# Kernel optimization log

Hardware: AMD Instinct MI355X
Metric: run time of the kernel (lower is better)

## Reference

```python
import jax, jax.numpy as jnp
import numpy as np

N, C, CI, H, W = 64, 512, 256, 12, 4
EPS = 1e-5


def _conv1x1(v, w, b=None):
    # v: [n, cin, h, w], w: [cout, cin]
    o = jnp.einsum('nchw,oc->nohw', v, w)
    if b is not None:
        o = o + b[None, :, None, None]
    return o


def _layernorm(v, g, b):
    # normalize over (C, H, W) per sample, affine params shaped [C, H, W]
    mu = v.mean(axis=(1, 2, 3), keepdims=True)
    var = v.var(axis=(1, 2, 3), keepdims=True)
    return (v - mu) / jnp.sqrt(var + EPS) * g[None] + b[None]


def setup_inputs() -> dict:
    key = jax.random.key(0)
    ks = jax.random.split(key, 12)
    s = 0.02
    return {
        'x': jax.random.normal(ks[0], (N, C, H, W), dtype=jnp.float32),
        'theta_w': jax.random.normal(ks[1], (CI, C), dtype=jnp.float32) * s,
        'theta_b': jnp.zeros((CI,), dtype=jnp.float32),
        'phi_w': jax.random.normal(ks[2], (CI, C), dtype=jnp.float32) * s,
        'phi_b': jnp.zeros((CI,), dtype=jnp.float32),
        'conv1_w': jax.random.normal(ks[3], (C, C), dtype=jnp.float32) * s,
        'conv2_w': jax.random.normal(ks[4], (C, C), dtype=jnp.float32) * s,
        'ln1_g': jnp.ones((C, H, W), dtype=jnp.float32),
        'ln1_b': jnp.zeros((C, H, W), dtype=jnp.float32),
        'ln2_g': jnp.ones((C, H, W), dtype=jnp.float32),
        'ln2_b': jnp.zeros((C, H, W), dtype=jnp.float32),
    }


def reference(x, theta_w, theta_b, phi_w, phi_b, conv1_w, conv2_w,
              ln1_g, ln1_b, ln2_g, ln2_b):
    n = x.shape[0]
    hw = H * W
    # 1x1 conv projections (conv is per-sample, so compute once on the N nodes
    # instead of on the N^2 gathered copies -- identical math)
    theta = _conv1x1(x, theta_w, theta_b)          # [N, CI, H, W]  (gallery proj)
    phi = _conv1x1(x, phi_w, phi_b)                # [N, CI, H, W]  (query proj)
    # MaxPool2d(2,2) on phi -> [N, CI, 6, 2] -> [N, CI, 12]
    phi_p = phi.reshape(n, CI, H // 2, 2, W // 2, 2).max(axis=(3, 5))
    phi_p = phi_p.reshape(n, CI, -1)               # [N, CI, 12]
    t = theta.reshape(n, CI, hw).transpose(0, 2, 1)  # [N, HW, CI]
    # f[i, j] = theta(x[j]) @ pooled phi(x[i]), norm='size' divides by 12
    f = jnp.einsum('jsc,icm->ijsm', t, phi_p) / phi_p.shape[-1]  # [Nq, Ng, HW, 12]
    m = f.max(axis=-1)                             # [Nq, Ng, HW]; max instead of softmax-sum
    # all-pairs layout p = i*N + j: qs[p] = i, gs[p] = j (torch.where row-major)
    gs = jnp.tile(jnp.arange(n), n)                # [N*N]
    # masked gallery image z = x[gs] * attention map, then scatter_add over gs
    z = x[gs] * m.reshape(n * n, 1, H, W)          # [N*N, C, H, W]
    x2 = jax.ops.segment_sum(z, gs, num_segments=n)
    # postprocessing (dropouts are identity at p=0)
    x = x2 + x                                     # res1
    x = _layernorm(x, ln1_g, ln1_b)
    h = _conv1x1(jax.nn.relu(_conv1x1(x, conv1_w)), conv2_w)
    x = x + h                                      # res2
    x = _layernorm(x, ln2_g, ln2_b)
    return x
```

## Files before the change

### kernel.cpp

```cpp
#include <hip/hip_runtime.h>
#include <hip/hip_bf16.h>

#define NN 64
#define CC 512
#define HW 48
#define LNSZ (CC * HW)

typedef __attribute__((ext_vector_type(8))) short bf16x8;
typedef __attribute__((ext_vector_type(4))) float floatx4;

static const size_t WB_OFF  = 0;
static const size_t BC_OFF  = 393216;
static const size_t XB_OFF  = 393728;
static const size_t YB_OFF  = 1180160;
static const size_t UB_OFF  = 1966592;
static const size_t TH_OFF  = 2753024;
static const size_t PP_OFF  = 3146240;
static const size_t PROJ_OFF= 3244544;
static const size_t DD_OFF  = 4817408;
static const size_t SS_OFF  = 7176704;
static const size_t YY_OFF  = 7179776;
static const size_t UU_OFF  = 8752640;
static const size_t HH_OFF  = 10325504;
static const size_t VV_OFF  = 11898368;
static const size_t ST1_OFF = 13471232;
static const size_t ST2_OFF = 13472256;

__device__ __forceinline__ void block_reduce2(float& sum, float& sq) {
  const int lane = threadIdx.x & 63, w = threadIdx.x >> 6;
#pragma unroll
  for (int off = 32; off > 0; off >>= 1) {
    sum += __shfl_down(sum, off, 64);
    sq  += __shfl_down(sq, off, 64);
  }
  __shared__ float rs[4], rq[4];
  if (lane == 0) { rs[w] = sum; rq[w] = sq; }
  __syncthreads();
  if (threadIdx.x == 0) {
    sum = rs[0] + rs[1] + rs[2] + rs[3];
    sq  = rq[0] + rq[1] + rq[2] + rq[3];
  }
}

__global__ __launch_bounds__(256) void prep_w(
    const float* __restrict__ tw, const float* __restrict__ pw,
    const float* __restrict__ c1, const float* __restrict__ c2,
    const float* __restrict__ tb, const float* __restrict__ pb,
    __hip_bfloat16* __restrict__ Wb, float* __restrict__ bcat) {
  int g = blockIdx.x * 256 + threadIdx.x;
  float v;
  if (g < 131072)      v = tw[g];
  else if (g < 262144) v = pw[g - 131072];
  else if (g < 524288) v = c1[g - 262144];
  else                 v = c2[g - 524288];
  Wb[g] = __float2bfloat16(v);
  if (g < 512) bcat[g] = g < 256 ? tb[g] : pb[g - 256];
}

__global__ __launch_bounds__(256) void tr_bf16(
    const float* __restrict__ in, __hip_bfloat16* __restrict__ out,
    int in_nstride, int out_nstride, int rowstr) {
  const int c0 = blockIdx.x * 128;
  const int n  = blockIdx.y;
  const int t  = threadIdx.x;
  __shared__ float ts[128 * 49];
  const float* src = in + (size_t)n * in_nstride + (size_t)c0 * HW;
#pragma unroll
  for (int k = 0; k < 6; ++k) {
    int idx = t + k * 256;
    float4 v = ((const float4*)src)[idx];
    int c = idx / 12, sq = (idx % 12) * 4;
    float* d = ts + c * 49 + sq;
    d[0] = v.x; d[1] = v.y; d[2] = v.z; d[3] = v.w;
  }
  __syncthreads();
  __hip_bfloat16* dst = out + (size_t)n * out_nstride + c0;
#pragma unroll
  for (int k = 0; k < 12; ++k) {
    int idx = t + k * 256;
    int s = idx >> 6, cp = idx & 63;
    __hip_bfloat162 p;
    p.x = __float2bfloat16(ts[(cp * 2) * 49 + s]);
    p.y = __float2bfloat16(ts[(cp * 2 + 1) * 49 + s]);
    *(__hip_bfloat162*)(dst + (size_t)s * rowstr + cp * 2) = p;
  }
}

__global__ __launch_bounds__(256) void gemm_conv(
    const __hip_bfloat16* __restrict__ Wb, const __hip_bfloat16* __restrict__ inb,
    const float* __restrict__ bias, float* __restrict__ out, int relu) {
  const int oc = blockIdx.x, n = blockIdx.y;
  const int w = threadIdx.x >> 6, lane = threadIdx.x & 63;
  const int c16 = lane & 15, quad = lane >> 4;
  const int obase = oc * 128 + w * 32;

  const __hip_bfloat16* A0 = Wb + (size_t)(obase + c16) * 512 + quad * 8;
  const __hip_bfloat16* A1 = A0 + 16 * 512;
  const __hip_bfloat16* B0 = inb + (size_t)n * LNSZ + (size_t)c16 * 512 + quad * 8;

  floatx4 zero = {0.f, 0.f, 0.f, 0.f};
  floatx4 acc[2][3];
#pragma unroll
  for (int i = 0; i < 2; ++i)
#pragma unroll
    for (int j = 0; j < 3; ++j) acc[i][j] = zero;

  bf16x8 a[2], b[3];
  a[0] = *(const bf16x8*)(A0);
  a[1] = *(const bf16x8*)(A1);
  b[0] = *(const bf16x8*)(B0);
  b[1] = *(const bf16x8*)(B0 + 16 * 512);
  b[2] = *(const bf16x8*)(B0 + 32 * 512);

  for (int k = 0; k < 480; k += 32) {
    bf16x8 an[2], bn[3];
    const int k2 = k + 32;
    an[0] = *(const bf16x8*)(A0 + k2);
    an[1] = *(const bf16x8*)(A1 + k2);
    bn[0] = *(const bf16x8*)(B0 + k2);
    bn[1] = *(const bf16x8*)(B0 + 16 * 512 + k2);
    bn[2] = *(const bf16x8*)(B0 + 32 * 512 + k2);
#pragma unroll
    for (int i = 0; i < 2; ++i)
#pragma unroll
      for (int j = 0; j < 3; ++j)
        acc[i][j] = __builtin_amdgcn_mfma_f32_16x16x32_bf16(a[i], b[j],
                                                            acc[i][j], 0, 0, 0);
    a[0] = an[0]; a[1] = an[1];
    b[0] = bn[0]; b[1] = bn[1]; b[2] = bn[2];
  }
#pragma unroll
  for (int i = 0; i < 2; ++i)
#pragma unroll
    for (int j = 0; j < 3; ++j)
      acc[i][j] = __builtin_amdgcn_mfma_f32_16x16x32_bf16(a[i], b[j],
                                                          acc[i][j], 0, 0, 0);

  float* on = out + (size_t)n * LNSZ;
#pragma unroll
  for (int i = 0; i < 2; ++i) {
#pragma unroll
    for (int r = 0; r < 4; ++r) {
      const int o = obase + i * 16 + quad * 4 + r;
      const float bv = bias ? bias[o] : 0.f;
#pragma unroll
      for (int j = 0; j < 3; ++j) {
        float v = acc[i][j][r] + bv;
        if (relu) v = fmaxf(v, 0.f);
        on[(size_t)o * HW + j * 16 + c16] = v;
      }
    }
  }
}

__global__ __launch_bounds__(256) void make_pp(
    const float* __restrict__ proj, __hip_bfloat16* __restrict__ Pp) {
  int g = blockIdx.x * 256 + threadIdx.x;
  int ci = g & 255;
  int rest = g >> 8;
  int m = rest % 12, i = rest / 12;
  int sb = (m >> 1) * 8 + (m & 1) * 2;
  const float* row = proj + (size_t)i * LNSZ + (size_t)(256 + ci) * HW;
  float2 p0 = *(const float2*)(row + sb);
  float2 p1 = *(const float2*)(row + sb + 4);
  float mx = fmaxf(fmaxf(p0.x, p0.y), fmaxf(p1.x, p1.y));
  Pp[g] = __float2bfloat16(mx);
}

__global__ __launch_bounds__(256) void dgemm_mfma(
    const __hip_bfloat16* __restrict__ A, const __hip_bfloat16* __restrict__ B,
    float* __restrict__ D) {
  const int bn = blockIdx.x * 48;
  const int w = threadIdx.x >> 6, lane = threadIdx.x & 63;
  const int c16 = lane & 15, quad = lane >> 4;
  const int bm = blockIdx.y * 128 + w * 32;

  const __hip_bfloat16* A0 = A + (size_t)(bm + c16) * 256 + quad * 8;
  const __hip_bfloat16* A1 = A0 + 16 * 256;
  const __hip_bfloat16* Bp = B + (size_t)(bn + c16) * 256 + quad * 8;

  floatx4 zero = {0.f, 0.f, 0.f, 0.f};
  floatx4 acc[2][3];
#pragma unroll
  for (int i = 0; i < 2; ++i)
#pragma unroll
    for (int j = 0; j < 3; ++j) acc[i][j] = zero;

#pragma unroll 2
  for (int k = 0; k < 256; k += 32) {
    bf16x8 a0 = *(const bf16x8*)(A0 + k);
    bf16x8 a1 = *(const bf16x8*)(A1 + k);
    bf16x8 b0 = *(const bf16x8*)(Bp + k);
    bf16x8 b1 = *(const bf16x8*)(Bp + 16 * 256 + k);
    bf16x8 b2 = *(const bf16x8*)(Bp + 32 * 256 + k);
    acc[0][0] = __builtin_amdgcn_mfma_f32_16x16x32_bf16(a0, b0, acc[0][0], 0, 0, 0);
    acc[0][1] = __builtin_amdgcn_mfma_f32_16x16x32_bf16(a0, b1, acc[0][1], 0, 0, 0);
    acc[0][2] = __builtin_amdgcn_mfma_f32_16x16x32_bf16(a0, b2, acc[0][2], 0, 0, 0);
    acc[1][0] = __builtin_amdgcn_mfma_f32_16x16x32_bf16(a1, b0, acc[1][0], 0, 0, 0);
    acc[1][1] = __builtin_amdgcn_mfma_f32_16x16x32_bf16(a1, b1, acc[1][1], 0, 0, 0);
    acc[1][2] = __builtin_amdgcn_mfma_f32_16x16x32_bf16(a1, b2, acc[1][2], 0, 0, 0);
  }

#pragma unroll
  for (int i = 0; i < 2; ++i)
#pragma unroll
    for (int r = 0; r < 4; ++r) {
      const int row = bm + i * 16 + quad * 4 + r;
#pragma unroll
      for (int j = 0; j < 3; ++j)
        D[(size_t)row * 768 + bn + j * 16 + c16] = acc[i][j][r];
    }
}

__global__ __launch_bounds__(256) void reduce_D(const float* __restrict__ D,
                                                float* __restrict__ S) {
  int w = threadIdx.x >> 6;
  int lane = threadIdx.x & 63;
  int row = blockIdx.x * 4 + w;
  const float* dr = D + (size_t)row * 768 + lane * 12;
  float4 a = *(const float4*)dr;
  float4 b = *(const float4*)(dr + 4);
  float4 c = *(const float4*)(dr + 8);
  float mx = a.x;
  mx = fmaxf(mx, a.y); mx = fmaxf(mx, a.z); mx = fmaxf(mx, a.w);
  mx = fmaxf(mx, b.x); mx = fmaxf(mx, b.y); mx = fmaxf(mx, b.z); mx = fmaxf(mx, b.w);
  mx = fmaxf(mx, c.x); mx = fmaxf(mx, c.y); mx = fmaxf(mx, c.z); mx = fmaxf(mx, c.w);
#pragma unroll
  for (int off = 32; off > 0; off >>= 1) mx += __shfl_down(mx, off, 64);
  if (lane == 0) S[row] = mx * (1.0f / 12.0f);
}

__global__ __launch_bounds__(256) void ln1_stats(
    const float* __restrict__ x, const float* __restrict__ S,
    float2* __restrict__ stats) {
  const int ch = blockIdx.x, n = blockIdx.y, t = threadIdx.x;
  __shared__ float sS[HW];
  if (t < HW) sS[t] = 1.0f + S[n * HW + t];
  __syncthreads();
  const float* xn = x + (size_t)n * LNSZ;
  float sum = 0.f, sq = 0.f;
#pragma unroll
  for (int k = 0; k < 3; ++k) {
    const int off = ch * 3072 + t * 4 + k * 1024;
    const int s0 = off % HW;
    float4 xv = *(const float4*)(xn + off);
    float e0 = xv.x * sS[s0];
    float e1 = xv.y * sS[s0 + 1];
    float e2 = xv.z * sS[s0 + 2];
    float e3 = xv.w * sS[s0 + 3];
    sum += (e0 + e1) + (e2 + e3);
    sq  += (e0 * e0 + e1 * e1) + (e2 * e2 + e3 * e3);
  }
  block_reduce2(sum, sq);
  if (t == 0) stats[n * 8 + ch] = make_float2(sum, sq);
}

__global__ __launch_bounds__(256) void ln1_norm(
    const float* __restrict__ x, const float* __restrict__ S,
    const float2* __restrict__ stats, const float* __restrict__ g,
    const float* __restrict__ b, float* __restrict__ y) {
  const int ch = blockIdx.x, n = blockIdx.y, t = threadIdx.x;
  __shared__ float sS[HW];
  __shared__ float smu, srstd;
  if (t < HW) sS[t] = 1.0f + S[n * HW + t];
  if (t == 0) {
    float s1 = 0.f, s2 = 0.f;
#pragma unroll
    for (int k = 0; k < 8; ++k) {
      float2 p = stats[n * 8 + k];
      s1 += p.x; s2 += p.y;
    }
    float mu = s1 * (1.0f / LNSZ);
    float var = s2 * (1.0f / LNSZ) - mu * mu;
    smu = mu;
    srstd = 1.0f / sqrtf(var + 1e-5f);
  }
  __syncthreads();
  const float mu = smu, rstd = srstd;
  const float* xn = x + (size_t)n * LNSZ;
  float* yn = y + (size_t)n * LNSZ;
#pragma unroll
  for (int k = 0; k < 3; ++k) {
    const int off = ch * 3072 + t * 4 + k * 1024;
    const int s0 = off % HW;
    float4 xv = *(const float4*)(xn + off);
    float4 gv = *(const float4*)(g + off);
    float4 bv = *(const float4*)(b + off);
    float4 o;
    o.x = (xv.x * sS[s0]     - mu) * rstd * gv.x + bv.x;
    o.y = (xv.y * sS[s0 + 1] - mu) * rstd * gv.y + bv.y;
    o.z = (xv.z * sS[s0 + 2] - mu) * rstd * gv.z + bv.z;
    o.w = (xv.w * sS[s0 + 3] - mu) * rstd * gv.w + bv.w;
    *(float4*)(yn + off) = o;
  }
}

__global__ __launch_bounds__(256) void ln2_stats(
    const float* __restrict__ y, const float* __restrict__ h,
    float2* __restrict__ stats, float* __restrict__ v) {
  const int ch = blockIdx.x, n = blockIdx.y, t = threadIdx.x;
  const size_t base = (size_t)n * LNSZ;
  float sum = 0.f, sq = 0.f;
#pragma unroll
  for (int k = 0; k < 3; ++k) {
    const int off = ch * 3072 + t * 4 + k * 1024;
    float4 yv = *(const float4*)(y + base + off);
    float4 hv = *(const float4*)(h + base + off);
    float v0 = yv.x + hv.x, v1 = yv.y + hv.y;
    float v2 = yv.z + hv.z, v3 = yv.w + hv.w;
    float4 o = make_float4(v0, v1, v2, v3);
    *(float4*)(v + base + off) = o;
    sum += (v0 + v1) + (v2 + v3);
    sq  += (v0 * v0 + v1 * v1) + (v2 * v2 + v3 * v3);
  }
  block_reduce2(sum, sq);
  if (t == 0) stats[n * 8 + ch] = make_float2(sum, sq);
}

__global__ __launch_bounds__(256) void ln2_norm(
    const float* __restrict__ v, const float2* __restrict__ stats,
    const float* __restrict__ g2, const float* __restrict__ b2,
    float* __restrict__ out) {
  const int ch = blockIdx.x, n = blockIdx.y, t = threadIdx.x;
  __shared__ float smu, srstd;
  if (t == 0) {
    float s1 = 0.f, s2 = 0.f;
#pragma unroll
    for (int k = 0; k < 8; ++k) {
      float2 p = stats[n * 8 + k];
      s1 += p.x; s2 += p.y;
    }
    float mu = s1 * (1.0f / LNSZ);
    float var = s2 * (1.0f / LNSZ) - mu * mu;
    smu = mu;
    srstd = 1.0f / sqrtf(var + 1e-5f);
  }
  __syncthreads();
  const float mu = smu, rstd = srstd;
  const float* vn = v + (size_t)n * LNSZ;
  float* on = out + (size_t)n * LNSZ;
#pragma unroll
  for (int k = 0; k < 3; ++k) {
    const int off = ch * 3072 + t * 4 + k * 1024;
    float4 vv = *(const float4*)(vn + off);
    float4 gv = *(const float4*)(g2 + off);
    float4 bv = *(const float4*)(b2 + off);
    float4 o;
    o.x = (vv.x - mu) * rstd * gv.x + bv.x;
    o.y = (vv.y - mu) * rstd * gv.y + bv.y;
    o.z = (vv.z - mu) * rstd * gv.z + bv.z;
    o.w = (vv.w - mu) * rstd * gv.w + bv.w;
    *(float4*)(on + off) = o;
  }
}

extern "C" void kernel_launch(void* const* d_in, const int* in_sizes, int n_in,
                              void* d_out, int out_size, void* d_ws, size_t ws_size,
                              hipStream_t stream) {
  const float* x   = (const float*)d_in[0];
  const float* tw  = (const float*)d_in[1];
  const float* tb  = (const float*)d_in[2];
  const float* pw  = (const float*)d_in[3];
  const float* pb  = (const float*)d_in[4];
  const float* c1w = (const float*)d_in[5];
  const float* c2w = (const float*)d_in[6];
  const float* g1  = (const float*)d_in[7];
  const float* b1  = (const float*)d_in[8];
  const float* g2  = (const float*)d_in[9];
  const float* b2  = (const float*)d_in[10];

  float* ws = (float*)d_ws;
  __hip_bfloat16* Wb = (__hip_bfloat16*)(ws + WB_OFF);
  float* bcat        = ws + BC_OFF;
  __hip_bfloat16* xb = (__hip_bfloat16*)(ws + XB_OFF);
  __hip_bfloat16* yb = (__hip_bfloat16*)(ws + YB_OFF);
  __hip_bfloat16* ub = (__hip_bfloat16*)(ws + UB_OFF);
  __hip_bfloat16* Th = (__hip_bfloat16*)(ws + TH_OFF);
  __hip_bfloat16* Pp = (__hip_bfloat16*)(ws + PP_OFF);
  float* proj = ws + PROJ_OFF;
  float* D    = ws + DD_OFF;
  float* S    = ws + SS_OFF;
  float* y    = ws + YY_OFF;
  float* u    = ws + UU_OFF;
  float* h    = ws + HH_OFF;
  float* v    = ws + VV_OFF;
  float2* st1 = (float2*)(ws + ST1_OFF);
  float2* st2 = (float2*)(ws + ST2_OFF);
  float* out  = (float*)d_out;

  prep_w<<<3072, 256, 0, stream>>>(tw, pw, c1w, c2w, tb, pb, Wb, bcat);
  tr_bf16<<<dim3(4, NN), 256, 0, stream>>>(x, xb, LNSZ, LNSZ, 512);
  gemm_conv<<<dim3(4, NN), 256, 0, stream>>>(Wb, xb, bcat, proj, 0);
  tr_bf16<<<dim3(2, NN), 256, 0, stream>>>(proj, Th, LNSZ, 48 * 256, 256);
  make_pp<<<768, 256, 0, stream>>>(proj, Pp);
  dgemm_mfma<<<dim3(16, 24), 256, 0, stream>>>(Th, Pp, D);
  reduce_D<<<768, 256, 0, stream>>>(D, S);
  ln1_stats<<<dim3(8, NN), 256, 0, stream>>>(x, S, st1);
  ln1_norm<<<dim3(8, NN), 256, 0, stream>>>(x, S, st1, g1, b1, y);
  tr_bf16<<<dim3(4, NN), 256, 0, stream>>>(y, yb, LNSZ, LNSZ, 512);
  gemm_conv<<<dim3(4, NN), 256, 0, stream>>>(Wb + 512 * 512, yb, nullptr, u, 1);
  tr_bf16<<<dim3(4, NN), 256, 0, stream>>>(u, ub, LNSZ, LNSZ, 512);
  gemm_conv<<<dim3(4, NN), 256, 0, stream>>>(Wb + 1024 * 512, ub, nullptr, h, 0);
  ln2_stats<<<dim3(8, NN), 256, 0, stream>>>(y, h, st2, v);
  ln2_norm<<<dim3(8, NN), 256, 0, stream>>>(v, st2, g2, b2, out);
}
```

Before: 161.3 us.

## Fuse pipeline stages: bf16 GEMM outputs, fused max-reduce, LN stats, residual epilogue

Measured after the change: 141.1 us, median of 2. -12.5%, faster.

```diff
diff --git a/kernel.cpp b/kernel.cpp
--- a/kernel.cpp
+++ b/kernel.cpp
@@ -9,22 +9,21 @@
 typedef __attribute__((ext_vector_type(8))) short bf16x8;
 typedef __attribute__((ext_vector_type(4))) float floatx4;
 
-static const size_t WB_OFF  = 0;
-static const size_t BC_OFF  = 393216;
-static const size_t XB_OFF  = 393728;
-static const size_t YB_OFF  = 1180160;
-static const size_t UB_OFF  = 1966592;
-static const size_t TH_OFF  = 2753024;
-static const size_t PP_OFF  = 3146240;
-static const size_t PROJ_OFF= 3244544;
-static const size_t DD_OFF  = 4817408;
-static const size_t SS_OFF  = 7176704;
-static const size_t YY_OFF  = 7179776;
-static const size_t UU_OFF  = 8752640;
-static const size_t HH_OFF  = 10325504;
-static const size_t VV_OFF  = 11898368;
-static const size_t ST1_OFF = 13471232;
-static const size_t ST2_OFF = 13472256;
+static const size_t WB_OFF   = 0;
+static const size_t BC_OFF   = 393216;
+static const size_t S_OFF    = 393728;
+static const size_t SMU_OFF  = 396800;
+static const size_t SRS_OFF  = 396864;
+static const size_t CXP_OFF  = 396928;
+static const size_t CX2_OFF  = 409216;
+static const size_t ST2_OFF  = 421504;
+static const size_t XB_OFF   = 422016;
+static const size_t TP_OFF   = 1208448;
+static const size_t YB_OFF   = 1994880;
+static const size_t UB_OFF   = 2781312;
+static const size_t PP_OFF   = 3567744;
+static const size_t YY_OFF   = 3666048;
+static const size_t VV_OFF   = 5238912;
 
 __device__ __forceinline__ void block_reduce2(float& sum, float& sq) {
   const int lane = threadIdx.x & 63, w = threadIdx.x >> 6;
@@ -46,7 +45,8 @@
     const float* __restrict__ tw, const float* __restrict__ pw,
     const float* __restrict__ c1, const float* __restrict__ c2,
     const float* __restrict__ tb, const float* __restrict__ pb,
-    __hip_bfloat16* __restrict__ Wb, float* __restrict__ bcat) {
+    __hip_bfloat16* __restrict__ Wb, float* __restrict__ bcat,
+    float* __restrict__ S) {
   int g = blockIdx.x * 256 + threadIdx.x;
   float v;
   if (g < 131072)      v = tw[g];
@@ -55,16 +55,18 @@
   else                 v = c2[g - 524288];
   Wb[g] = __float2bfloat16(v);
   if (g < 512) bcat[g] = g < 256 ? tb[g] : pb[g - 256];
-}
-
-__global__ __launch_bounds__(256) void tr_bf16(
-    const float* __restrict__ in, __hip_bfloat16* __restrict__ out,
-    int in_nstride, int out_nstride, int rowstr) {
-  const int c0 = blockIdx.x * 128;
+  if (g < 3072) S[g] = 0.f;
+}
+
+__global__ __launch_bounds__(256) void trx_stats(
+    const float* __restrict__ x, __hip_bfloat16* __restrict__ xb,
+    float* __restrict__ cxp, float* __restrict__ cx2p) {
+  const int bx = blockIdx.x;
   const int n  = blockIdx.y;
   const int t  = threadIdx.x;
   __shared__ float ts[128 * 49];
-  const float* src = in + (size_t)n * in_nstride + (size_t)c0 * HW;
+  __shared__ float ps[192], pq[192];
+  const float* src = x + (size_t)n * LNSZ + (size_t)bx * 128 * HW;
 #pragma unroll
   for (int k = 0; k < 6; ++k) {
     int idx = t + k * 256;
@@ -74,7 +76,17 @@
     d[0] = v.x; d[1] = v.y; d[2] = v.z; d[3] = v.w;
   }
   __syncthreads();
-  __hip_bfloat16* dst = out + (size_t)n * out_nstride + c0;
+  if (t < 192) {
+    int s = t % 48, q = t / 48;
+    float sum = 0.f, sq2 = 0.f;
+#pragma unroll
+    for (int c = q * 32; c < q * 32 + 32; ++c) {
+      float v = ts[c * 49 + s];
+      sum += v; sq2 += v * v;
+    }
+    ps[t] = sum; pq[t] = sq2;
+  }
+  __hip_bfloat16* dst = xb + (size_t)n * LNSZ + bx * 128;
 #pragma unroll
   for (int k = 0; k < 12; ++k) {
     int idx = t + k * 256;
@@ -82,13 +94,18 @@
     __hip_bfloat162 p;
     p.x = __float2bfloat16(ts[(cp * 2) * 49 + s]);
     p.y = __float2bfloat16(ts[(cp * 2 + 1) * 49 + s]);
-    *(__hip_bfloat162*)(dst + (size_t)s * rowstr + cp * 2) = p;
-  }
-}
-
-__global__ __launch_bounds__(256) void gemm_conv(
+    *(__hip_bfloat162*)(dst + (size_t)s * 512 + cp * 2) = p;
+  }
+  __syncthreads();
+  if (t < 48) {
+    cxp[((size_t)n * 4 + bx) * 48 + t] = ps[t] + ps[48 + t] + ps[96 + t] + ps[144 + t];
+    cx2p[((size_t)n * 4 + bx) * 48 + t] = pq[t] + pq[48 + t] + pq[96 + t] + pq[144 + t];
+  }
+}
+
+__global__ __launch_bounds__(256) void gemm_bf16out(
     const __hip_bfloat16* __restrict__ Wb, const __hip_bfloat16* __restrict__ inb,
-    const float* __restrict__ bias, float* __restrict__ out, int relu) {
+    const float* __restrict__ bias, __hip_bfloat16* __restrict__ outb, int relu) {
   const int oc = blockIdx.x, n = blockIdx.y;
   const int w = threadIdx.x >> 6, lane = threadIdx.x & 63;
   const int c16 = lane & 15, quad = lane >> 4;
@@ -136,47 +153,53 @@
       acc[i][j] = __builtin_amdgcn_mfma_f32_16x16x32_bf16(a[i], b[j],
                                                           acc[i][j], 0, 0, 0);
 
-  float* on = out + (size_t)n * LNSZ;
+  __hip_bfloat16* on = outb + (size_t)n * LNSZ;
 #pragma unroll
   for (int i = 0; i < 2; ++i) {
-#pragma unroll
-    for (int r = 0; r < 4; ++r) {
-      const int o = obase + i * 16 + quad * 4 + r;
-      const float bv = bias ? bias[o] : 0.f;
-#pragma unroll
-      for (int j = 0; j < 3; ++j) {
-        float v = acc[i][j][r] + bv;
+    const int o0 = obase + i * 16 + quad * 4;
+    float bv[4];
+#pragma unroll
+    for (int r = 0; r < 4; ++r) bv[r] = bias ? bias[o0 + r] : 0.f;
+#pragma unroll
+    for (int j = 0; j < 3; ++j) {
+      const int s = j * 16 + c16;
+      union { short4 s4; __hip_bfloat16 h[4]; } u;
+#pragma unroll
+      for (int r = 0; r < 4; ++r) {
+        float v = acc[i][j][r] + bv[r];
         if (relu) v = fmaxf(v, 0.f);
-        on[(size_t)o * HW + j * 16 + c16] = v;
+        u.h[r] = __float2bfloat16(v);
       }
+      *(short4*)(on + (size_t)s * 512 + o0) = u.s4;
     }
   }
 }
 
 __global__ __launch_bounds__(256) void make_pp(
-    const float* __restrict__ proj, __hip_bfloat16* __restrict__ Pp) {
+    const __hip_bfloat16* __restrict__ ThPhi, __hip_bfloat16* __restrict__ Pp) {
   int g = blockIdx.x * 256 + threadIdx.x;
   int ci = g & 255;
   int rest = g >> 8;
   int m = rest % 12, i = rest / 12;
   int sb = (m >> 1) * 8 + (m & 1) * 2;
-  const float* row = proj + (size_t)i * LNSZ + (size_t)(256 + ci) * HW;
-  float2 p0 = *(const float2*)(row + sb);
-  float2 p1 = *(const float2*)(row + sb + 4);
-  float mx = fmaxf(fmaxf(p0.x, p0.y), fmaxf(p1.x, p1.y));
+  const __hip_bfloat16* base = ThPhi + (size_t)i * LNSZ + 256 + ci;
+  float mx = __bfloat162float(base[(size_t)(sb + 0) * 512]);
+  mx = fmaxf(mx, __bfloat162float(base[(size_t)(sb + 1) * 512]));
+  mx = fmaxf(mx, __bfloat162float(base[(size_t)(sb + 4) * 512]));
+  mx = fmaxf(mx, __bfloat162float(base[(size_t)(sb + 5) * 512]));
   Pp[g] = __float2bfloat16(mx);
 }
 
-__global__ __launch_bounds__(256) void dgemm_mfma(
+__global__ __launch_bounds__(256) void dgemm_fused(
     const __hip_bfloat16* __restrict__ A, const __hip_bfloat16* __restrict__ B,
-    float* __restrict__ D) {
+    float* __restrict__ S) {
   const int bn = blockIdx.x * 48;
   const int w = threadIdx.x >> 6, lane = threadIdx.x & 63;
   const int c16 = lane & 15, quad = lane >> 4;
   const int bm = blockIdx.y * 128 + w * 32;
 
-  const __hip_bfloat16* A0 = A + (size_t)(bm + c16) * 256 + quad * 8;
-  const __hip_bfloat16* A1 = A0 + 16 * 256;
+  const __hip_bfloat16* A0 = A + (size_t)(bm + c16) * 512 + quad * 8;
+  const __hip_bfloat16* A1 = A0 + 16 * 512;
   const __hip_bfloat16* Bp = B + (size_t)(bn + c16) * 256 + quad * 8;
 
   floatx4 zero = {0.f, 0.f, 0.f, 0.f};
@@ -201,73 +224,188 @@
     acc[1][2] = __builtin_amdgcn_mfma_f32_16x16x32_bf16(a1, b2, acc[1][2], 0, 0, 0);
   }
 
-#pragma unroll
-  for (int i = 0; i < 2; ++i)
-#pragma unroll
-    for (int r = 0; r < 4; ++r) {
-      const int row = bm + i * 16 + quad * 4 + r;
-#pragma unroll
-      for (int j = 0; j < 3; ++j)
-        D[(size_t)row * 768 + bn + j * 16 + c16] = acc[i][j][r];
-    }
-}
-
-__global__ __launch_bounds__(256) void reduce_D(const float* __restrict__ D,
-                                                float* __restrict__ S) {
-  int w = threadIdx.x >> 6;
-  int lane = threadIdx.x & 63;
-  int row = blockIdx.x * 4 + w;
-  const float* dr = D + (size_t)row * 768 + lane * 12;
-  float4 a = *(const float4*)dr;
-  float4 b = *(const float4*)(dr + 4);
-  float4 c = *(const float4*)(dr + 8);
-  float mx = a.x;
-  mx = fmaxf(mx, a.y); mx = fmaxf(mx, a.z); mx = fmaxf(mx, a.w);
-  mx = fmaxf(mx, b.x); mx = fmaxf(mx, b.y); mx = fmaxf(mx, b.z); mx = fmaxf(mx, b.w);
-  mx = fmaxf(mx, c.x); mx = fmaxf(mx, c.y); mx = fmaxf(mx, c.z); mx = fmaxf(mx, c.w);
-#pragma unroll
-  for (int off = 32; off > 0; off >>= 1) mx += __shfl_down(mx, off, 64);
-  if (lane == 0) S[row] = mx * (1.0f / 12.0f);
-}
-
-__global__ __launch_bounds__(256) void ln1_stats(
+  __shared__ float red[4 * 48 * 33];
+  float* rw = red + w * (48 * 33);
+#pragma unroll
+  for (int i = 0; i < 2; ++i)
+#pragma unroll
+    for (int j = 0; j < 3; ++j)
+#pragma unroll
+      for (int r = 0; r < 4; ++r)
+        rw[(j * 16 + c16) * 33 + (i * 16 + quad * 4 + r)] = acc[i][j][r];
+  __syncthreads();
+  if (lane < 32) {
+    float sum = 0.f;
+#pragma unroll
+    for (int grp = 0; grp < 4; ++grp) {
+      float mx = rw[(grp * 12) * 33 + lane];
+#pragma unroll
+      for (int m = 1; m < 12; ++m)
+        mx = fmaxf(mx, rw[(grp * 12 + m) * 33 + lane]);
+      sum += mx;
+    }
+    atomicAdd(&S[bm + lane], sum * (1.0f / 12.0f));
+  }
+}
+
+__global__ __launch_bounds__(64) void ln1_finish(
+    const float* __restrict__ S, const float* __restrict__ cxp,
+    const float* __restrict__ cx2p, float* __restrict__ smu,
+    float* __restrict__ srstd) {
+  const int n = blockIdx.x, lane = threadIdx.x;
+  float sum = 0.f, sq = 0.f;
+  if (lane < 48) {
+    float a = 1.0f + S[n * 48 + lane];
+    float c1 = 0.f, c2 = 0.f;
+#pragma unroll
+    for (int ch = 0; ch < 4; ++ch) {
+      c1 += cxp[((size_t)n * 4 + ch) * 48 + lane];
+      c2 += cx2p[((size_t)n * 4 + ch) * 48 + lane];
+    }
+    sum = a * c1;
+    sq = a * a * c2;
+  }
+#pragma unroll
+  for (int off = 32; off > 0; off >>= 1) {
+    sum += __shfl_down(sum, off, 64);
+    sq  += __shfl_down(sq, off, 64);
+  }
+  if (lane == 0) {
+    float mu = sum * (1.0f / LNSZ);
+    float var = sq * (1.0f / LNSZ) - mu * mu;
+    smu[n] = mu;
+    srstd[n] = 1.0f / sqrtf(var + 1e-5f);
+  }
+}
+
+__global__ __launch_bounds__(256) void ln1_norm_tr(
     const float* __restrict__ x, const float* __restrict__ S,
-    float2* __restrict__ stats) {
-  const int ch = blockIdx.x, n = blockIdx.y, t = threadIdx.x;
+    const float* __restrict__ smu, const float* __restrict__ srstd,
+    const float* __restrict__ g, const float* __restrict__ b,
+    float* __restrict__ y, __hip_bfloat16* __restrict__ yb) {
+  const int bx = blockIdx.x, n = blockIdx.y, t = threadIdx.x;
+  __shared__ float ts[128 * 49];
   __shared__ float sS[HW];
   if (t < HW) sS[t] = 1.0f + S[n * HW + t];
   __syncthreads();
-  const float* xn = x + (size_t)n * LNSZ;
+  const float mu = smu[n], rstd = srstd[n];
+  const size_t chunk = (size_t)bx * 6144;
+  const float* xn = x + (size_t)n * LNSZ + chunk;
+  float* yn = y + (size_t)n * LNSZ + chunk;
+  const float* gp = g + chunk;
+  const float* bp = b + chunk;
+#pragma unroll
+  for (int k = 0; k < 6; ++k) {
+    int idx = t + k * 256;
+    int c = idx / 12, sq0 = (idx % 12) * 4;
+    float4 xv = ((const float4*)xn)[idx];
+    float4 gv = ((const float4*)gp)[idx];
+    float4 bv = ((const float4*)bp)[idx];
+    float4 o;
+    o.x = (xv.x * sS[sq0]     - mu) * rstd * gv.x + bv.x;
+    o.y = (xv.y * sS[sq0 + 1] - mu) * rstd * gv.y + bv.y;
+    o.z = (xv.z * sS[sq0 + 2] - mu) * rstd * gv.z + bv.z;
+    o.w = (xv.w * sS[sq0 + 3] - mu) * rstd * gv.w + bv.w;
+    ((float4*)yn)[idx] = o;
+    float* d = ts + c * 49 + sq0;
+    d[0] = o.x; d[1] = o.y; d[2] = o.z; d[3] = o.w;
+  }
+  __syncthreads();
+  __hip_bfloat16* dst = yb + (size_t)n * LNSZ + bx * 128;
+#pragma unroll
+  for (int k = 0; k < 12; ++k) {
+    int idx = t + k * 256;
+    int s = idx >> 6, cp = idx & 63;
+    __hip_bfloat162 p;
+    p.x = __float2bfloat16(ts[(cp * 2) * 49 + s]);
+    p.y = __float2bfloat16(ts[(cp * 2 + 1) * 49 + s]);
+    *(__hip_bfloat162*)(dst + (size_t)s * 512 + cp * 2) = p;
+  }
+}
+
+__global__ __launch_bounds__(256) void conv2_fused(
+    const __hip_bfloat16* __restrict__ Wb, const __hip_bfloat16* __restrict__ inb,
+    const float* __restrict__ y, float* __restrict__ v,
+    float2* __restrict__ stats2) {
+  const int oc = blockIdx.x, n = blockIdx.y;
+  const int w = threadIdx.x >> 6, lane = threadIdx.x & 63;
+  const int c16 = lane & 15, quad = lane >> 4;
+  const int obase = oc * 128 + w * 32;
+
+  const __hip_bfloat16* A0 = Wb + (size_t)(obase + c16) * 512 + quad * 8;
+  const __hip_bfloat16* A1 = A0 + 16 * 512;
+  const __hip_bfloat16* B0 = inb + (size_t)n * LNSZ + (size_t)c16 * 512 + quad * 8;
+
+  floatx4 zero = {0.f, 0.f, 0.f, 0.f};
+  floatx4 acc[2][3];
+#pragma unroll
+  for (int i = 0; i < 2; ++i)
+#pragma unroll
+    for (int j = 0; j < 3; ++j) acc[i][j] = zero;
+
+  bf16x8 a[2], b[3];
+  a[0] = *(const bf16x8*)(A0);
+  a[1] = *(const bf16x8*)(A1);
+  b[0] = *(const bf16x8*)(B0);
+  b[1] = *(const bf16x8*)(B0 + 16 * 512);
+  b[2] = *(const bf16x8*)(B0 + 32 * 512);
+
+  for (int k = 0; k < 480; k += 32) {
+    bf16x8 an[2], bn[3];
+    const int k2 = k + 32;
+    an[0] = *(const bf16x8*)(A0 + k2);
+    an[1] = *(const bf16x8*)(A1 + k2);
+    bn[0] = *(const bf16x8*)(B0 + k2);
+    bn[1] = *(const bf16x8*)(B0 + 16 * 512 + k2);
+    bn[2] = *(const bf16x8*)(B0 + 32 * 512 + k2);
+#pragma unroll
+    for (int i = 0; i < 2; ++i)
+#pragma unroll
+      for (int j = 0; j < 3; ++j)
+        acc[i][j] = __builtin_amdgcn_mfma_f32_16x16x32_bf16(a[i], b[j],
+                                                            acc[i][j], 0, 0, 0);
+    a[0] = an[0]; a[1] = an[1];
+    b[0] = bn[0]; b[1] = bn[1]; b[2] = bn[2];
+  }
+#pragma unroll
+  for (int i = 0; i < 2; ++i)
+#pragma unroll
+    for (int j = 0; j < 3; ++j)
+      acc[i][j] = __builtin_amdgcn_mfma_f32_16x16x32_bf16(a[i], b[j],
+                                                          acc[i][j], 0, 0, 0);
+
+  const float* yn = y + (size_t)n * LNSZ;
+  float* vn = v + (size_t)n * LNSZ;
   float sum = 0.f, sq = 0.f;
 #pragma unroll
-  for (int k = 0; k < 3; ++k) {
-    const int off = ch * 3072 + t * 4 + k * 1024;
-    const int s0 = off % HW;
-    float4 xv = *(const float4*)(xn + off);
-    float e0 = xv.x * sS[s0];
-    float e1 = xv.y * sS[s0 + 1];
-    float e2 = xv.z * sS[s0 + 2];
-    float e3 = xv.w * sS[s0 + 3];
-    sum += (e0 + e1) + (e2 + e3);
-    sq  += (e0 * e0 + e1 * e1) + (e2 * e2 + e3 * e3);
-  }
+  for (int i = 0; i < 2; ++i)
+#pragma unroll
+    for (int r = 0; r < 4; ++r) {
+      const int o = obase + i * 16 + quad * 4 + r;
+#pragma unroll
+      for (int j = 0; j < 3; ++j) {
+        const int s = j * 16 + c16;
+        float val = acc[i][j][r] + yn[(size_t)o * HW + s];
+        vn[(size_t)o * HW + s] = val;
+        sum += val;
+        sq += val * val;
+      }
+    }
   block_reduce2(sum, sq);
-  if (t == 0) stats[n * 8 + ch] = make_float2(sum, sq);
-}
-
-__global__ __launch_bounds__(256) void ln1_norm(
-    const float* __restrict__ x, const float* __restrict__ S,
-    const float2* __restrict__ stats, const float* __restrict__ g,
-    const float* __restrict__ b, float* __restrict__ y) {
-  const int ch = blockIdx.x, n = blockIdx.y, t = threadIdx.x;
-  __shared__ float sS[HW];
+  if (threadIdx.x == 0) stats2[n * 4 + oc] = make_float2(sum, sq);
+}
+
+__global__ __launch_bounds__(256) void ln2_norm(
+    const float* __restrict__ v, const float2* __restrict__ stats2,
+    const float* __restrict__ g2, const float* __restrict__ b2,
+    float* __restrict__ out) {
+  const int bx = blockIdx.x, n = blockIdx.y, t = threadIdx.x;
   __shared__ float smu, srstd;
-  if (t < HW) sS[t] = 1.0f + S[n * HW + t];
   if (t == 0) {
     float s1 = 0.f, s2 = 0.f;
 #pragma unroll
-    for (int k = 0; k < 8; ++k) {
-      float2 p = stats[n * 8 + k];
+    for (int k = 0; k < 4; ++k) {
+      float2 p = stats2[n * 4 + k];
       s1 += p.x; s2 += p.y;
     }
     float mu = s1 * (1.0f / LNSZ);
@@ -277,80 +415,23 @@
   }
   __syncthreads();
   const float mu = smu, rstd = srstd;
-  const float* xn = x + (size_t)n * LNSZ;
-  float* yn = y + (size_t)n * LNSZ;
-#pragma unroll
-  for (int k = 0; k < 3; ++k) {
-    const int off = ch * 3072 + t * 4 + k * 1024;
-    const int s0 = off % HW;
-    float4 xv = *(const float4*)(xn + off);
-    float4 gv = *(const float4*)(g + off);
-    float4 bv = *(const float4*)(b + off);
-    float4 o;
-    o.x = (xv.x * sS[s0]     - mu) * rstd * gv.x + bv.x;
-    o.y = (xv.y * sS[s0 + 1] - mu) * rstd * gv.y + bv.y;
-    o.z = (xv.z * sS[s0 + 2] - mu) * rstd * gv.z + bv.z;
-    o.w = (xv.w * sS[s0 + 3] - mu) * rstd * gv.w + bv.w;
-    *(float4*)(yn + off) = o;
-  }
-}
-
-__global__ __launch_bounds__(256) void ln2_stats(
-    const float* __restrict__ y, const float* __restrict__ h,
-    float2* __restrict__ stats, float* __restrict__ v) {
-  const int ch = blockIdx.x, n = blockIdx.y, t = threadIdx.x;
-  const size_t base = (size_t)n * LNSZ;
-  float sum = 0.f, sq = 0.f;
-#pragma unroll
-  for (int k = 0; k < 3; ++k) {
-    const int off = ch * 3072 + t * 4 + k * 1024;
-    float4 yv = *(const float4*)(y + base + off);
-    float4 hv = *(const float4*)(h + base + off);
-    float v0 = yv.x + hv.x, v1 = yv.y + hv.y;
-    float v2 = yv.z + hv.z, v3 = yv.w + hv.w;
-    float4 o = make_float4(v0, v1, v2, v3);
-    *(float4*)(v + base + off) = o;
-    sum += (v0 + v1) + (v2 + v3);
-    sq  += (v0 * v0 + v1 * v1) + (v2 * v2 + v3 * v3);
-  }
-  block_reduce2(sum, sq);
-  if (t == 0) stats[n * 8 + ch] = make_float2(sum, sq);
-}
-
-__global__ __launch_bounds__(256) void ln2_norm(
-    const float* __restrict__ v, const float2* __restrict__ stats,
-    const float* __restrict__ g2, const float* __restrict__ b2,
-    float* __restrict__ out) {
-  const int ch = blockIdx.x, n = blockIdx.y, t = threadIdx.x;
-  __shared__ float smu, srstd;
-  if (t == 0) {
-    float s1 = 0.f, s2 = 0.f;
-#pragma unroll
-    for (int k = 0; k < 8; ++k) {
-      float2 p = stats[n * 8 + k];
-      s1 += p.x; s2 += p.y;
-    }
-    float mu = s1 * (1.0f / LNSZ);
-    float var = s2 * (1.0f / LNSZ) - mu * mu;
-    smu = mu;
-    srstd = 1.0f / sqrtf(var + 1e-5f);
-  }
-  __syncthreads();
-  const float mu = smu, rstd = srstd;
-  const float* vn = v + (size_t)n * LNSZ;
-  float* on = out + (size_t)n * LNSZ;
-#pragma unroll
-  for (int k = 0; k < 3; ++k) {
-    const int off = ch * 3072 + t * 4 + k * 1024;
-    float4 vv = *(const float4*)(vn + off);
-    float4 gv = *(const float4*)(g2 + off);
-    float4 bv = *(const float4*)(b2 + off);
+  const size_t chunk = (size_t)bx * 6144;
+  const float* vn = v + (size_t)n * LNSZ + chunk;
+  float* on = out + (size_t)n * LNSZ + chunk;
+  const float* gp = g2 + chunk;
+  const float* bp = b2 + chunk;
+#pragma unroll
+  for (int k = 0; k < 6; ++k) {
+    int idx = t + k * 256;
+    float4 vv = ((const float4*)vn)[idx];
+    float4 gv = ((const float4*)gp)[idx];
+    float4 bv = ((const float4*)bp)[idx];
     float4 o;
     o.x = (vv.x - mu) * rstd * gv.x + bv.x;
     o.y = (vv.y - mu) * rstd * gv.y + bv.y;
     o.z = (vv.z - mu) * rstd * gv.z + bv.z;
     o.w = (vv.w - mu) * rstd * gv.w + bv.w;
-    *(float4*)(on + off) = o;
+    ((float4*)on)[idx] = o;
   }
 }
 
@@ -372,35 +453,29 @@
   float* ws = (float*)d_ws;
   __hip_bfloat16* Wb = (__hip_bfloat16*)(ws + WB_OFF);
   float* bcat        = ws + BC_OFF;
+  float* S           = ws + S_OFF;
+  float* smu         = ws + SMU_OFF;
+  float* srstd       = ws + SRS_OFF;
+  float* cxp         = ws + CXP_OFF;
+  float* cx2p        = ws + CX2_OFF;
+  float2* st2        = (float2*)(ws + ST2_OFF);
   __hip_bfloat16* xb = (__hip_bfloat16*)(ws + XB_OFF);
+  __hip_bfloat16* tp = (__hip_bfloat16*)(ws + TP_OFF);
   __hip_bfloat16* yb = (__hip_bfloat16*)(ws + YB_OFF);
   __hip_bfloat16* ub = (__hip_bfloat16*)(ws + UB_OFF);
-  __hip_bfloat16* Th = (__hip_bfloat16*)(ws + TH_OFF);
   __hip_bfloat16* Pp = (__hip_bfloat16*)(ws + PP_OFF);
-  float* proj = ws + PROJ_OFF;
-  float* D    = ws + DD_OFF;
-  float* S    = ws + SS_OFF;
-  float* y    = ws + YY_OFF;
-  float* u    = ws + UU_OFF;
-  float* h    = ws + HH_OFF;
-  float* v    = ws + VV_OFF;
-  float2* st1 = (float2*)(ws + ST1_OFF);
-  float2* st2 = (float2*)(ws + ST2_OFF);
-  float* out  = (float*)d_out;
-
-  prep_w<<<3072, 256, 0, stream>>>(tw, pw, c1w, c2w, tb, pb, Wb, bcat);
-  tr_bf16<<<dim3(4, NN), 256, 0, stream>>>(x, xb, LNSZ, LNSZ, 512);
-  gemm_conv<<<dim3(4, NN), 256, 0, stream>>>(Wb, xb, bcat, proj, 0);
-  tr_bf16<<<dim3(2, NN), 256, 0, stream>>>(proj, Th, LNSZ, 48 * 256, 256);
-  make_pp<<<768, 256, 0, stream>>>(proj, Pp);
-  dgemm_mfma<<<dim3(16, 24), 256, 0, stream>>>(Th, Pp, D);
-  reduce_D<<<768, 256, 0, stream>>>(D, S);
-  ln1_stats<<<dim3(8, NN), 256, 0, stream>>>(x, S, st1);
-  ln1_norm<<<dim3(8, NN), 256, 0, stream>>>(x, S, st1, g1, b1, y);
-  tr_bf16<<<dim3(4, NN), 256, 0, stream>>>(y, yb, LNSZ, LNSZ, 512);
-  gemm_conv<<<dim3(4, NN), 256, 0, stream>>>(Wb + 512 * 512, yb, nullptr, u, 1);
-  tr_bf16<<<dim3(4, NN), 256, 0, stream>>>(u, ub, LNSZ, LNSZ, 512);
-  gemm_conv<<<dim3(4, NN), 256, 0, stream>>>(Wb + 1024 * 512, ub, nullptr, h, 0);
-  ln2_stats<<<dim3(8, NN), 256, 0, stream>>>(y, h, st2, v);
-  ln2_norm<<<dim3(8, NN), 256, 0, stream>>>(v, st2, g2, b2, out);
-}
+  float* y           = ws + YY_OFF;
+  float* v           = ws + VV_OFF;
+  float* out         = (float*)d_out;
+
+  prep_w<<<3072, 256, 0, stream>>>(tw, pw, c1w, c2w, tb, pb, Wb, bcat, S);
+  trx_stats<<<dim3(4, NN), 256, 0, stream>>>(x, xb, cxp, cx2p);
+  gemm_bf16out<<<dim3(4, NN), 256, 0, stream>>>(Wb, xb, bcat, tp, 0);
+  make_pp<<<768, 256, 0, stream>>>(tp, Pp);
+  dgemm_fused<<<dim3(16, 24), 256, 0, stream>>>(tp, Pp, S);
+  ln1_finish<<<NN, 64, 0, stream>>>(S, cxp, cx2p, smu, srstd);
+  ln1_norm_tr<<<dim3(4, NN), 256, 0, stream>>>(x, S, smu, srstd, g1, b1, y, yb);
+  gemm_bf16out<<<dim3(4, NN), 256, 0, stream>>>(Wb + 512 * 512, yb, nullptr, ub, 1);
+  conv2_fused<<<dim3(4, NN), 256, 0, stream>>>(Wb + 1024 * 512, ub, y, v, st2);
+  ln2_norm<<<dim3(4, NN), 256, 0, stream>>>(v, st2, g2, b2, out);
+}
```
